# Performance work log

Hardware: AMD Instinct MI355X
Metric: run time of the kernel (lower is better)

## Reference

```python
import jax, jax.numpy as jnp
import numpy as np

NUM_EMBEDDINGS = 512
EMBEDDING_DIM = 128

def setup_inputs() -> dict:
    key = jax.random.key(0)
    k1, k2 = jax.random.split(key)
    z_e = jax.random.normal(k1, (32, EMBEDDING_DIM, 64, 64), dtype=jnp.float32)
    embedding = jax.random.normal(k2, (NUM_EMBEDDINGS, EMBEDDING_DIM), dtype=jnp.float32)
    return {"z_e": z_e, "embedding": embedding}

def reference(z_e, embedding):
    B, C, H, W = z_e.shape
    # (B,C,H,W) -> (N, C) with N = B*H*W
    z_flat = jnp.transpose(z_e, (0, 2, 3, 1)).reshape(-1, C)
    # squared L2 distance via expansion: ||z||^2 - 2 z.E^T + ||E||^2  (avoids (N,K,C) intermediate)
    z_sq = jnp.sum(z_flat * z_flat, axis=-1, keepdims=True)          # (N,1)
    e_sq = jnp.sum(embedding * embedding, axis=-1)                    # (K,)
    dist = z_sq - 2.0 * jnp.einsum('nc,kc->nk', z_flat, embedding) + e_sq  # (N,K)
    indices = jnp.argmin(dist, axis=1)                                # (N,)
    z_q = embedding[indices].reshape(B, H, W, C)                      # gather
    return jnp.transpose(z_q, (0, 3, 1, 2))                           # (B,C,H,W)
```

## Files before the change

kernel.cpp:

```cpp
#include <hip/hip_runtime.h>
#include <float.h>

#define NUM_EMB 512
#define DIM     128
#define HWX     4096
#define NPOS    (32 * 4096)
#define MARGIN  0.35f
#define FULLPAD 0.01f

#define WS_E16   ((size_t)33554432)
#define WS_ESQ   ((size_t)33685504)
#define WS_WL    ((size_t)34211840)
#define WS_CNT   ((size_t)34736128)
#define WS_NEED  ((size_t)34736384)

using half8 = __attribute__((ext_vector_type(8))) _Float16;
using f32x4 = __attribute__((ext_vector_type(4))) float;

__global__ void prep_kernel(const float* __restrict__ emb, _Float16* __restrict__ e16,
                            float* __restrict__ esq, int* __restrict__ cnt) {
    int k = blockIdx.x * blockDim.x + threadIdx.x;
    if (k == 0) { cnt[0] = 0; cnt[1] = 0; }
    if (k < NUM_EMB) {
        const float4* row = (const float4*)(emb + (size_t)k * DIM);
        _Float16* dst = e16 + (size_t)k * DIM;
        float s0 = 0.f, s1 = 0.f, s2 = 0.f, s3 = 0.f;
        #pragma unroll
        for (int c = 0; c < DIM / 4; ++c) {
            float4 v = row[c];
            s0 = fmaf(v.x, v.x, s0);
            s1 = fmaf(v.y, v.y, s1);
            s2 = fmaf(v.z, v.z, s2);
            s3 = fmaf(v.w, v.w, s3);
            dst[4 * c + 0] = (_Float16)v.x;
            dst[4 * c + 1] = (_Float16)v.y;
            dst[4 * c + 2] = (_Float16)v.z;
            dst[4 * c + 3] = (_Float16)v.w;
        }
        esq[k] = (s0 + s1) + (s2 + s3);
    }
}

__global__ __launch_bounds__(256) void gemm_argmin(const float* __restrict__ z,
                                                   const _Float16* __restrict__ e16,
                                                   const float* __restrict__ esq,
                                                   const float* __restrict__ emb,
                                                   float* __restrict__ out,
                                                   int* __restrict__ wl,
                                                   int* __restrict__ cnt) {
    __shared__ __align__(16) char Ash[128 * 272];
    __shared__ float mB1[2][128];
    __shared__ float mB2[2][128];
    __shared__ float mB3[2][128];
    __shared__ int   ish[128];

    int t = threadIdx.x;
    int lane = t & 63, wave = t >> 6;
    int wm = wave & 1, wn = wave >> 1;
    int quad = lane >> 4, l15 = lane & 15;
    int n0 = blockIdx.x * 128;
    int bb = n0 >> 12;
    int hw0 = n0 & 4095;

    {
        int g = t & 31, cq = t >> 5;
        int hw = hw0 + 4 * g;
        const float* zp = z + (size_t)bb * DIM * HWX + (size_t)cq * 16 * HWX + hw;
        char* arow0 = Ash + (4 * g) * 272;
        int xr = g & 7;
        #pragma unroll
        for (int k = 0; k < 2; ++k) {
            float4 v[8];
            #pragma unroll
            for (int c = 0; c < 8; ++c)
                v[c] = *(const float4*)(zp + (size_t)(k * 8 + c) * HWX);
            int slotb = ((2 * cq + k) ^ xr) * 16;
            #pragma unroll
            for (int j = 0; j < 4; ++j) {
                half8 hv;
                #pragma unroll
                for (int c = 0; c < 8; ++c) {
                    float f = (j == 0) ? v[c].x : (j == 1) ? v[c].y
                            : (j == 2) ? v[c].z : v[c].w;
                    hv[c] = (_Float16)f;
                }
                *(half8*)(arow0 + j * 272 + slotb) = hv;
            }
        }
    }
    __syncthreads();

    float b1[16], b2[16], b3[16];
    #pragma unroll
    for (int s = 0; s < 16; ++s) { b1[s] = 3.0e38f; b2[s] = 3.0e38f; b3[s] = 3.0e38f; }

    const char* abase = Ash + (wm * 64 + l15) * 272 + (quad ^ (l15 >> 2)) * 16;
    const char* ebase = (const char*)e16 + ((size_t)(wn * 32 + l15) << 8) + quad * 16;
    const float* eqb  = esq + wn * 32 + l15;

    for (int tile = 0; tile < 8; ++tile) {
        half8 bf[2][4];
        {
            const char* eb = ebase + (size_t)tile * 64 * 256;
            #pragma unroll
            for (int nt = 0; nt < 2; ++nt)
                #pragma unroll
                for (int kc = 0; kc < 4; ++kc)
                    bf[nt][kc] = *(const half8*)(eb + nt * 4096 + kc * 64);
        }
        float es0 = eqb[tile * 64];
        float es1 = eqb[tile * 64 + 16];

        f32x4 acc[4][2];
        #pragma unroll
        for (int mt = 0; mt < 4; ++mt)
            #pragma unroll
            for (int nt = 0; nt < 2; ++nt)
                acc[mt][nt] = (f32x4){0.f, 0.f, 0.f, 0.f};

        #pragma unroll
        for (int kc = 0; kc < 4; ++kc) {
            half8 af[4];
            #pragma unroll
            for (int mt = 0; mt < 4; ++mt)
                af[mt] = *(const half8*)(abase + mt * (16 * 272) + ((kc ^ (mt & 1)) * 64));
            #pragma unroll
            for (int mt = 0; mt < 4; ++mt)
                #pragma unroll
                for (int nt = 0; nt < 2; ++nt)
                    acc[mt][nt] = __builtin_amdgcn_mfma_f32_16x16x32_f16(af[mt], bf[nt][kc], acc[mt][nt], 0, 0, 0);
        }

        #pragma unroll
        for (int nt = 0; nt < 2; ++nt) {
            unsigned code = (unsigned)(tile * 64 + wn * 32 + nt * 16 + l15);
            float es = nt ? es1 : es0;
            #pragma unroll
            for (int mt = 0; mt < 4; ++mt)
                #pragma unroll
                for (int r = 0; r < 4; ++r) {
                    int s = mt * 4 + r;
                    float sc = fmaf(-2.0f, acc[mt][nt][r], es);
                    float p = __uint_as_float((__float_as_uint(sc) & 0xFFFFFE00u) | code);
                    float t1 = fmaxf(b1[s], p);
                    b1[s] = fminf(b1[s], p);
                    float t2 = fmaxf(b2[s], t1);
                    b2[s] = fminf(b2[s], t1);
                    b3[s] = fminf(b3[s], t2);
                }
        }
    }

    #pragma unroll
    for (int d = 1; d < 16; d <<= 1) {
        #pragma unroll
        for (int s = 0; s < 16; ++s) {
            float o1 = __shfl_xor(b1[s], d, 64);
            float o2 = __shfl_xor(b2[s], d, 64);
            float o3 = __shfl_xor(b3[s], d, 64);
            float u1 = fmaxf(b1[s], o1);
            b1[s] = fminf(b1[s], o1);
            float l2 = fminf(b2[s], o2);
            float w  = fmaxf(u1, l2);
            b2[s] = fminf(u1, l2);
            b3[s] = fminf(fminf(b3[s], o3), w);
        }
    }
    if (l15 == 0) {
        #pragma unroll
        for (int s = 0; s < 16; ++s) {
            int m = wm * 64 + (s >> 2) * 16 + quad * 4 + (s & 3);
            mB1[wn][m] = b1[s];
            mB2[wn][m] = b2[s];
            mB3[wn][m] = b3[s];
        }
    }
    __syncthreads();
    if (t < 128) {
        float a1 = mB1[0][t], c1 = mB1[1][t];
        float a2 = mB2[0][t], c2 = mB2[1][t];
        float a3 = mB3[0][t], c3 = mB3[1][t];
        float u1 = fmaxf(a1, c1);
        float m1 = fminf(a1, c1);
        float l2 = fminf(a2, c2);
        float m2 = fminf(u1, l2);
        float m3 = fminf(fminf(a3, c3), fmaxf(u1, l2));
        int ix1 = (int)(__float_as_uint(m1) & 511u);
        int ix2 = (int)(__float_as_uint(m2) & 511u);
        ish[t] = ix1 | (ix2 << 9);
        if (m3 - m1 < MARGIN + FULLPAD) {
            int p = atomicAdd(cnt, 1);
            wl[p] = n0 + t;
        }
    }
    __syncthreads();

    {
        int g = t & 31, cq = t >> 5;
        int hw = hw0 + 4 * g;
        const float* zp = z + (size_t)bb * DIM * HWX + (size_t)cq * 16 * HWX + hw;
        int ii[4];
        #pragma unroll
        for (int j = 0; j < 4; ++j) ii[j] = ish[4 * g + j];
        float d1[4] = {0.f, 0.f, 0.f, 0.f};
        float d2[4] = {0.f, 0.f, 0.f, 0.f};
        #pragma unroll
        for (int k = 0; k < 2; ++k) {
            float4 v[8];
            #pragma unroll
            for (int c = 0; c < 8; ++c)
                v[c] = *(const float4*)(zp + (size_t)(k * 8 + c) * HWX);
            #pragma unroll
            for (int j = 0; j < 4; ++j) {
                const float* e1p = emb + (size_t)(ii[j] & 511) * DIM + cq * 16 + k * 8;
                const float* e2p = emb + (size_t)((ii[j] >> 9) & 511) * DIM + cq * 16 + k * 8;
                float4 p0 = *(const float4*)(e1p), p1 = *(const float4*)(e1p + 4);
                float4 q0 = *(const float4*)(e2p), q1 = *(const float4*)(e2p + 4);
                float e1c[8] = {p0.x, p0.y, p0.z, p0.w, p1.x, p1.y, p1.z, p1.w};
                float e2c[8] = {q0.x, q0.y, q0.z, q0.w, q1.x, q1.y, q1.z, q1.w};
                #pragma unroll
                for (int c = 0; c < 8; ++c) {
                    float zc = (j == 0) ? v[c].x : (j == 1) ? v[c].y
                             : (j == 2) ? v[c].z : v[c].w;
                    d1[j] = fmaf(zc, e1c[c], d1[j]);
                    d2[j] = fmaf(zc, e2c[c], d2[j]);
                }
            }
        }
        float2* part = (float2*)Ash;
        #pragma unroll
        for (int j = 0; j < 4; ++j)
            part[(4 * g + j) * 9 + cq] = make_float2(d1[j], d2[j]);
    }
    __syncthreads();
    if (t < 128) {
        int ii = ish[t];
        int i1 = ii & 511, i2 = (ii >> 9) & 511;
        const float2* pr = (const float2*)Ash + (size_t)t * 9;
        float d1 = 0.f, d2 = 0.f;
        #pragma unroll
        for (int cq = 0; cq < 8; ++cq) {
            float2 pv = pr[cq];
            d1 += pv.x;
            d2 += pv.y;
        }
        float s1 = fmaf(-2.f, d1, esq[i1]);
        float s2 = fmaf(-2.f, d2, esq[i2]);
        bool take2 = (s2 < s1) || (s2 == s1 && i2 < i1);
        ish[t] = take2 ? i2 : i1;
    }
    __syncthreads();

    {
        int g = t & 31, cq = t >> 5;
        int hw = hw0 + 4 * g;
        int i0 = ish[4 * g + 0], i1v = ish[4 * g + 1];
        int i2 = ish[4 * g + 2], i3 = ish[4 * g + 3];
        const float4* e0 = (const float4*)(emb + (size_t)i0 * DIM) + cq * 4;
        const float4* e1 = (const float4*)(emb + (size_t)i1v * DIM) + cq * 4;
        const float4* e2 = (const float4*)(emb + (size_t)i2 * DIM) + cq * 4;
        const float4* e3 = (const float4*)(emb + (size_t)i3 * DIM) + cq * 4;
        float* ob = out + (size_t)bb * DIM * HWX + (size_t)cq * 16 * HWX + hw;
        #pragma unroll
        for (int cc = 0; cc < 4; ++cc) {
            float4 r0 = e0[cc], r1 = e1[cc], r2 = e2[cc], r3 = e3[cc];
            *(float4*)(ob + (size_t)(4 * cc + 0) * HWX) = (float4){r0.x, r1.x, r2.x, r3.x};
            *(float4*)(ob + (size_t)(4 * cc + 1) * HWX) = (float4){r0.y, r1.y, r2.y, r3.y};
            *(float4*)(ob + (size_t)(4 * cc + 2) * HWX) = (float4){r0.z, r1.z, r2.z, r3.z};
            *(float4*)(ob + (size_t)(4 * cc + 3) * HWX) = (float4){r0.w, r1.w, r2.w, r3.w};
        }
    }
}

__global__ __launch_bounds__(256) void refine_kernel(const float* __restrict__ z,
                                                     const float* __restrict__ emb,
                                                     const float* __restrict__ esq,
                                                     const int* __restrict__ wl,
                                                     const int* __restrict__ cnt,
                                                     float* __restrict__ out) {
    __shared__ __align__(16) float zsh[16][132];
    __shared__ __align__(16) float esh[64][132];
    __shared__ float rs[16][16];
    __shared__ int   ri[16][16];
    __shared__ int   nsh[16];
    __shared__ int   ksh[16];

    int t = threadIdx.x;
    int te = t & 15, tc = t >> 4;
    int count = *cnt;

    for (int base = blockIdx.x * 16; base < count; base += gridDim.x * 16) {
        {
            int e = t >> 4, d = t & 15;
            int ge = base + e;
            if (ge > count - 1) ge = count - 1;
            int n = wl[ge];
            if (d == 0) nsh[e] = n;
            int b = n >> 12, hw = n & 4095;
            const float* zp = z + (size_t)b * DIM * HWX + hw;
            #pragma unroll
            for (int jj = 0; jj < 8; ++jj)
                zsh[e][d + 16 * jj] = zp[(size_t)(d + 16 * jj) * HWX];
        }

        float bs = 3.0e38f; int bk = 0;

        for (int tile = 0; tile < 8; ++tile) {
            __syncthreads();
            {
                const float4* gsrc = (const float4*)(emb + (size_t)tile * 64 * DIM);
                #pragma unroll
                for (int jj = 0; jj < 8; ++jj) {
                    int f = jj * 256 + t;
                    int k = f >> 5, q = f & 31;
                    float4 v = gsrc[f];
                    *(float4*)&esh[k][q * 4] = v;
                }
                if (t < 64) esh[t][128] = esq[tile * 64 + t];
            }
            __syncthreads();

            float acc[4] = {0.f, 0.f, 0.f, 0.f};
            #pragma unroll 4
            for (int c4 = 0; c4 < 32; ++c4) {
                float4 zv = *(const float4*)&zsh[te][c4 * 4];
                #pragma unroll
                for (int j = 0; j < 4; ++j) {
                    float4 ev = *(const float4*)&esh[tc * 4 + j][c4 * 4];
                    acc[j] = fmaf(zv.x, ev.x, acc[j]);
                    acc[j] = fmaf(zv.y, ev.y, acc[j]);
                    acc[j] = fmaf(zv.z, ev.z, acc[j]);
                    acc[j] = fmaf(zv.w, ev.w, acc[j]);
                }
            }
            #pragma unroll
            for (int j = 0; j < 4; ++j) {
                int k = tile * 64 + tc * 4 + j;
                float es = esh[tc * 4 + j][128];
                float s = fmaf(-2.f, acc[j], es);
                if (s < bs) { bs = s; bk = k; }
            }
        }
        __syncthreads();
        rs[te][tc] = bs; ri[te][tc] = bk;
        __syncthreads();
        if (t < 16) {
            float s = rs[t][0]; int k = ri[t][0];
            #pragma unroll
            for (int q = 1; q < 16; ++q) {
                float s2 = rs[t][q]; int k2 = ri[t][q];
                bool take = (s2 < s) || (s2 == s && k2 < k);
                s = take ? s2 : s;
                k = take ? k2 : k;
            }
            ksh[t] = k;
        }
        __syncthreads();
        {
            int e = t >> 4, d = t & 15;
            int n = nsh[e];
            int b = n >> 12, hw = n & 4095;
            int kk = ksh[e];
            const float* er = emb + (size_t)kk * DIM;
            float* ob = out + (size_t)b * DIM * HWX + hw;
            #pragma unroll
            for (int jj = 0; jj < 8; ++jj)
                ob[(size_t)(d + 16 * jj) * HWX] = er[d + 16 * jj];
        }
        __syncthreads();
    }
}

__global__ void esq_kernel(const float* __restrict__ emb, float* __restrict__ e_sq) {
    int k = blockIdx.x * blockDim.x + threadIdx.x;
    if (k < NUM_EMB) {
        const float4* row = (const float4*)(emb + k * DIM);
        float s0 = 0.f, s1 = 0.f, s2 = 0.f, s3 = 0.f;
        #pragma unroll
        for (int c = 0; c < DIM / 4; ++c) {
            float4 v = row[c];
            s0 = fmaf(v.x, v.x, s0); s1 = fmaf(v.y, v.y, s1);
            s2 = fmaf(v.z, v.z, s2); s3 = fmaf(v.w, v.w, s3);
        }
        e_sq[k] = (s0 + s1) + (s2 + s3);
    }
}

__global__ __launch_bounds__(256) void vq_kernel(const float* __restrict__ z,
                                                 const float* __restrict__ emb,
                                                 const float* __restrict__ e_sq,
                                                 float* __restrict__ out) {
    int n = blockIdx.x * 256 + threadIdx.x;
    int b = n >> 12, hw = n & 4095;
    const float* zb = z + (size_t)b * DIM * HWX + hw;
    float zr[DIM];
    #pragma unroll
    for (int c = 0; c < DIM; ++c) zr[c] = zb[(size_t)c * HWX];
    float best = FLT_MAX; int besti = 0;
    for (int k = 0; k < NUM_EMB; ++k) {
        const float4* er = (const float4*)(emb + k * DIM);
        float d0 = 0.f, d1 = 0.f, d2 = 0.f, d3 = 0.f;
        #pragma unroll
        for (int c = 0; c < DIM / 4; ++c) {
            float4 e = er[c];
            d0 = fmaf(zr[4 * c + 0], e.x, d0);
            d1 = fmaf(zr[4 * c + 1], e.y, d1);
            d2 = fmaf(zr[4 * c + 2], e.z, d2);
            d3 = fmaf(zr[4 * c + 3], e.w, d3);
        }
        float s = e_sq[k] - 2.f * ((d0 + d1) + (d2 + d3));
        if (s < best) { best = s; besti = k; }
    }
    float* ob = out + (size_t)b * DIM * HWX + hw;
    const float4* sel = (const float4*)(emb + (size_t)besti * DIM);
    #pragma unroll
    for (int c4 = 0; c4 < DIM / 4; ++c4) {
        float4 v = sel[c4];
        ob[(size_t)(4 * c4 + 0) * HWX] = v.x;
        ob[(size_t)(4 * c4 + 1) * HWX] = v.y;
        ob[(size_t)(4 * c4 + 2) * HWX] = v.z;
        ob[(size_t)(4 * c4 + 3) * HWX] = v.w;
    }
}

extern "C" void kernel_launch(void* const* d_in, const int* in_sizes, int n_in,
                              void* d_out, int out_size, void* d_ws, size_t ws_size,
                              hipStream_t stream) {
    const float* z   = (const float*)d_in[0];
    const float* emb = (const float*)d_in[1];
    float* out = (float*)d_out;

    if (ws_size < WS_NEED) {
        float* e_sq = (float*)d_ws;
        esq_kernel<<<(NUM_EMB + 255) / 256, 256, 0, stream>>>(emb, e_sq);
        vq_kernel<<<NPOS / 256, 256, 0, stream>>>(z, emb, e_sq, out);
        return;
    }

    char* ws = (char*)d_ws;
    _Float16* e16 = (_Float16*)(ws + WS_E16);
    float*    esq = (float*)(ws + WS_ESQ);
    int*      wl  = (int*)(ws + WS_WL);
    int*      cnt = (int*)(ws + WS_CNT);

    prep_kernel<<<2, 256, 0, stream>>>(emb, e16, esq, cnt);
    gemm_argmin<<<NPOS / 128, 256, 0, stream>>>(z, e16, esq, emb, out, wl, cnt);
    refine_kernel<<<512, 256, 0, stream>>>(z, emb, esq, wl, cnt, out);
}
```

Measured before the change: 214.2 us.

## Restructure refine kernel to read embeddings from global with wave-shuffle argmin

The refine kernel no longer stages embedding tiles in shared memory behind repeated block barriers. Each wave now handles 4 positions, each lane covers 8 codebook entries read straight from global/L2, and the argmin is reduced with wave shuffles instead of a shared-memory pass. The grid grows from 512 to 1024 blocks. This removes barriers and LDS traffic but adds uncoalesced global embedding loads (each lane reads a different row) and more register pressure.

```diff
diff --git a/kernel.cpp b/kernel.cpp
--- a/kernel.cpp
+++ b/kernel.cpp
@@ -279,14 +279,10 @@
                                                      const int* __restrict__ cnt,
                                                      float* __restrict__ out) {
     __shared__ __align__(16) float zsh[16][132];
-    __shared__ __align__(16) float esh[64][132];
-    __shared__ float rs[16][16];
-    __shared__ int   ri[16][16];
-    __shared__ int   nsh[16];
-    __shared__ int   ksh[16];
-
-    int t = threadIdx.x;
-    int te = t & 15, tc = t >> 4;
+    __shared__ int nsh[16];
+    __shared__ int ksh[16];
+
+    int t = threadIdx.x, lane = t & 63, wave = t >> 6;
     int count = *cnt;
 
     for (int base = blockIdx.x * 16; base < count; base += gridDim.x * 16) {
@@ -302,58 +298,65 @@
             for (int jj = 0; jj < 8; ++jj)
                 zsh[e][d + 16 * jj] = zp[(size_t)(d + 16 * jj) * HWX];
         }
-
-        float bs = 3.0e38f; int bk = 0;
-
-        for (int tile = 0; tile < 8; ++tile) {
-            __syncthreads();
-            {
-                const float4* gsrc = (const float4*)(emb + (size_t)tile * 64 * DIM);
-                #pragma unroll
-                for (int jj = 0; jj < 8; ++jj) {
-                    int f = jj * 256 + t;
-                    int k = f >> 5, q = f & 31;
-                    float4 v = gsrc[f];
-                    *(float4*)&esh[k][q * 4] = v;
+        __syncthreads();
+
+        int e0 = wave * 4;
+        float acc[4][8];
+        #pragma unroll
+        for (int e = 0; e < 4; ++e)
+            #pragma unroll
+            for (int j = 0; j < 8; ++j) acc[e][j] = 0.f;
+
+        const float* ebase = emb + (size_t)lane * DIM;
+        #pragma unroll 4
+        for (int c4 = 0; c4 < 32; ++c4) {
+            float4 zv[4];
+            #pragma unroll
+            for (int e = 0; e < 4; ++e)
+                zv[e] = *(const float4*)&zsh[e0 + e][c4 * 4];
+            float4 ev[8];
+            #pragma unroll
+            for (int j = 0; j < 8; ++j)
+                ev[j] = *(const float4*)(ebase + (size_t)j * 64 * DIM + c4 * 4);
+            #pragma unroll
+            for (int e = 0; e < 4; ++e)
+                #pragma unroll
+                for (int j = 0; j < 8; ++j) {
+                    acc[e][j] = fmaf(zv[e].x, ev[j].x, acc[e][j]);
+                    acc[e][j] = fmaf(zv[e].y, ev[j].y, acc[e][j]);
+                    acc[e][j] = fmaf(zv[e].z, ev[j].z, acc[e][j]);
+                    acc[e][j] = fmaf(zv[e].w, ev[j].w, acc[e][j]);
                 }
-                if (t < 64) esh[t][128] = esq[tile * 64 + t];
+        }
+
+        float esv[8];
+        #pragma unroll
+        for (int j = 0; j < 8; ++j) esv[j] = esq[64 * j + lane];
+
+        float bs[4]; int bk[4];
+        #pragma unroll
+        for (int e = 0; e < 4; ++e) {
+            bs[e] = 3.0e38f; bk[e] = 0;
+            #pragma unroll
+            for (int j = 0; j < 8; ++j) {
+                float s = fmaf(-2.f, acc[e][j], esv[j]);
+                if (s < bs[e]) { bs[e] = s; bk[e] = 64 * j + lane; }
             }
-            __syncthreads();
-
-            float acc[4] = {0.f, 0.f, 0.f, 0.f};
-            #pragma unroll 4
-            for (int c4 = 0; c4 < 32; ++c4) {
-                float4 zv = *(const float4*)&zsh[te][c4 * 4];
-                #pragma unroll
-                for (int j = 0; j < 4; ++j) {
-                    float4 ev = *(const float4*)&esh[tc * 4 + j][c4 * 4];
-                    acc[j] = fmaf(zv.x, ev.x, acc[j]);
-                    acc[j] = fmaf(zv.y, ev.y, acc[j]);
-                    acc[j] = fmaf(zv.z, ev.z, acc[j]);
-                    acc[j] = fmaf(zv.w, ev.w, acc[j]);
-                }
+        }
+        #pragma unroll
+        for (int d = 1; d < 64; d <<= 1) {
+            #pragma unroll
+            for (int e = 0; e < 4; ++e) {
+                float os = __shfl_xor(bs[e], d, 64);
+                int   ok = __shfl_xor(bk[e], d, 64);
+                bool take = (os < bs[e]) || (os == bs[e] && ok < bk[e]);
+                bs[e] = take ? os : bs[e];
+                bk[e] = take ? ok : bk[e];
             }
-            #pragma unroll
-            for (int j = 0; j < 4; ++j) {
-                int k = tile * 64 + tc * 4 + j;
-                float es = esh[tc * 4 + j][128];
-                float s = fmaf(-2.f, acc[j], es);
-                if (s < bs) { bs = s; bk = k; }
-            }
-        }
-        __syncthreads();
-        rs[te][tc] = bs; ri[te][tc] = bk;
-        __syncthreads();
-        if (t < 16) {
-            float s = rs[t][0]; int k = ri[t][0];
-            #pragma unroll
-            for (int q = 1; q < 16; ++q) {
-                float s2 = rs[t][q]; int k2 = ri[t][q];
-                bool take = (s2 < s) || (s2 == s && k2 < k);
-                s = take ? s2 : s;
-                k = take ? k2 : k;
-            }
-            ksh[t] = k;
+        }
+        if (lane == 0) {
+            #pragma unroll
+            for (int e = 0; e < 4; ++e) ksh[e0 + e] = bk[e];
         }
         __syncthreads();
         {
@@ -445,5 +448,5 @@
 
     prep_kernel<<<2, 256, 0, stream>>>(emb, e16, esq, cnt);
     gemm_argmin<<<NPOS / 128, 256, 0, stream>>>(z, e16, esq, emb, out, wl, cnt);
-    refine_kernel<<<512, 256, 0, stream>>>(z, emb, esq, wl, cnt, out);
-}
+    refine_kernel<<<1024, 256, 0, stream>>>(z, emb, esq, wl, cnt, out);
+}
```

Result: no change. 212.3 us (-0.9%).
